# Kernel optimization log

Hardware: AMD Instinct MI355X
Metric: run time of the kernel (lower is better)

## Reference

```python
import jax, jax.numpy as jnp
import numpy as np

NUM_EXPERTS = 8
HIDDEN = 1024
INTER = 2048
TOKENS = 2048
TOP_K = 2


def setup_inputs() -> dict:
    key = jax.random.key(0)
    k1, k2, k3, k4, k5 = jax.random.split(key, 5)
    hidden_states = jax.random.normal(k1, (TOKENS, HIDDEN), dtype=jnp.float32)
    top_k_index = jax.random.randint(k2, (TOKENS, TOP_K), 0, NUM_EXPERTS, dtype=jnp.int64)
    top_k_weights = jax.random.uniform(k3, (TOKENS, TOP_K), dtype=jnp.float32)
    # parameters, scaled like typical init
    gate_up_proj = jax.random.normal(k4, (NUM_EXPERTS, 2 * INTER, HIDDEN), dtype=jnp.float32) * (HIDDEN ** -0.5)
    down_proj = jax.random.normal(k5, (NUM_EXPERTS, HIDDEN, INTER), dtype=jnp.float32) * (INTER ** -0.5)
    return {
        "hidden_states": hidden_states,
        "top_k_index": top_k_index,
        "top_k_weights": top_k_weights,
        "gate_up_proj": gate_up_proj,
        "down_proj": down_proj,
    }


def reference(hidden_states, top_k_index, top_k_weights, gate_up_proj, down_proj):
    # combine weights per (token, expert): w[t, e] = sum_k 1[idx[t,k]==e] * tw[t,k]
    one_hot = jax.nn.one_hot(top_k_index, NUM_EXPERTS, dtype=hidden_states.dtype)  # [T, K, E]
    combine = jnp.einsum("tke,tk->te", one_hot, top_k_weights)  # [T, E]

    out = jnp.zeros_like(hidden_states)
    # fixed small loop over experts (structural, not a data dim)
    for e in range(NUM_EXPERTS):
        gu = hidden_states @ gate_up_proj[e].T  # [T, 2I]
        gate, up = jnp.split(gu, 2, axis=-1)
        h = jax.nn.gelu(gate, approximate=True) * up  # gelu_pytorch_tanh
        y = h @ down_proj[e].T  # [T, H]
        out = out + y * combine[:, e][:, None]
    return out
```

## Files before the change

### kernel.cpp

```cpp
#include <hip/hip_runtime.h>
#include <stdint.h>

#define T_TOK  2048
#define HID    1024
#define INTERN 2048
#define NEXP   8
#define MAXPOS 5248

typedef __attribute__((ext_vector_type(8))) short          bf16x8;
typedef __attribute__((ext_vector_type(4))) float          f32x4;
typedef __attribute__((ext_vector_type(8))) unsigned short u16x8;
typedef __attribute__((ext_vector_type(4))) unsigned short u16x4;

__device__ __forceinline__ unsigned short f32_to_bf16(float f) {
  unsigned int u = __float_as_uint(f);
  unsigned int r = (u + 0x7FFFu + ((u >> 16) & 1u)) >> 16;
  return (unsigned short)r;
}

__device__ __forceinline__ float bf16_to_f32(unsigned short h) {
  unsigned int u = ((unsigned int)h) << 16;
  return __uint_as_float(u);
}

__device__ __forceinline__ void gload_lds16(const void* g, void* l) {
  __builtin_amdgcn_global_load_lds(
      (const __attribute__((address_space(1))) unsigned int*)g,
      (__attribute__((address_space(3))) unsigned int*)l, 16, 0, 0);
}

__device__ __forceinline__ u16x8 cvt8(float4 a, float4 b) {
  u16x8 w;
  w[0] = f32_to_bf16(a.x); w[1] = f32_to_bf16(a.y);
  w[2] = f32_to_bf16(a.z); w[3] = f32_to_bf16(a.w);
  w[4] = f32_to_bf16(b.x); w[5] = f32_to_bf16(b.y);
  w[6] = f32_to_bf16(b.z); w[7] = f32_to_bf16(b.w);
  return w;
}

#define WAIT_VM0()    asm volatile("s_waitcnt vmcnt(0)" ::: "memory")
#define WAIT_LGKM0()  asm volatile("s_waitcnt lgkmcnt(0)" ::: "memory")
#define SCHED_FENCE() __builtin_amdgcn_sched_barrier(0)

__global__ void route_kernel(const int* __restrict__ tki,
                             const float* __restrict__ tkw,
                             int* __restrict__ counts,
                             int* __restrict__ offsets,
                             int* __restrict__ tok_list,
                             float* __restrict__ w_list,
                             int* __restrict__ pos_map,
                             float* __restrict__ wgt_map) {
  __shared__ int scnt[NEXP];
  __shared__ int soff[NEXP];
  int tid = threadIdx.x;
  if (tid < NEXP) scnt[tid] = 0;
  __syncthreads();
  for (int t = tid; t < T_TOK; t += 256) {
    int e0 = tki[2 * t] & 7;
    int e1 = tki[2 * t + 1] & 7;
    float w0 = tkw[2 * t];
    float w1 = tkw[2 * t + 1];
    if (e0 == e1) {
      int p = atomicAdd(&scnt[e0], 1);
      tok_list[e0 * T_TOK + p] = t;
      w_list [e0 * T_TOK + p] = w0 + w1;
      pos_map[2 * t]     = (p << 3) | e0;
      wgt_map[2 * t]     = w0 + w1;
      pos_map[2 * t + 1] = -1;
      wgt_map[2 * t + 1] = 0.0f;
    } else {
      int p = atomicAdd(&scnt[e0], 1);
      tok_list[e0 * T_TOK + p] = t;
      w_list [e0 * T_TOK + p] = w0;
      pos_map[2 * t]     = (p << 3) | e0;
      wgt_map[2 * t]     = w0;
      int q = atomicAdd(&scnt[e1], 1);
      tok_list[e1 * T_TOK + q] = t;
      w_list [e1 * T_TOK + q] = w1;
      pos_map[2 * t + 1] = (q << 3) | e1;
      wgt_map[2 * t + 1] = w1;
    }
  }
  __syncthreads();
  if (tid == 0) {
    int acc = 0;
    for (int e = 0; e < NEXP; ++e) {
      counts[e]  = scnt[e];
      offsets[e] = acc;
      soff[e]    = acc;
      acc += ((scnt[e] + 127) >> 7) << 7;
    }
  }
  __syncthreads();
  for (int i = tid; i < 2 * T_TOK; i += 256) {
    int v = pos_map[i];
    if (v >= 0) pos_map[i] = soff[v & 7] + (v >> 3);
  }
}

__global__ void cvt_x_kernel(const float* __restrict__ x, unsigned short* __restrict__ xb) {
  int i = blockIdx.x * 256 + threadIdx.x;
  float4 v = ((const float4*)x)[i];
  u16x4 o;
  o[0] = f32_to_bf16(v.x); o[1] = f32_to_bf16(v.y);
  o[2] = f32_to_bf16(v.z); o[3] = f32_to_bf16(v.w);
  *((u16x4*)(xb + 4 * (size_t)i)) = o;
}

__global__ __launch_bounds__(256, 4)
void gemm1_kernel(const unsigned short* __restrict__ xb,
                  const float* __restrict__ gup,
                  const int* __restrict__ counts,
                  const int* __restrict__ offsets,
                  const int* __restrict__ tok_list,
                  unsigned short* __restrict__ hbuf) {
  int e  = blockIdx.z;
  int Ne = counts[e];
  int m0 = blockIdx.y * 128;
  if (m0 >= Ne) return;
  int n0  = blockIdx.x * 64;
  int off = offsets[e];

  __shared__ __align__(16) unsigned short As[2][4][128][8];
  __shared__ __align__(16) unsigned short Gs[2][4][64][8];
  __shared__ __align__(16) unsigned short Us[2][4][64][8];

  int tid  = threadIdx.x;
  int lane = tid & 63;
  int wave = tid >> 6;
  int wm = wave >> 1;
  int wn = wave & 1;

  int arow = tid & 127;
  int akg  = tid >> 7;
  int rg   = m0 + arow;
  int tok  = (rg < Ne) ? tok_list[e * T_TOK + rg] : 0;
  const unsigned short* asrc = xb + (size_t)tok * HID;

  int brow = tid >> 2;
  int bq   = tid & 3;
  const float* gsrc = gup + (size_t)e * (2 * INTERN) * HID + (size_t)(n0 + brow) * HID + bq * 8;
  const float* usrc = gsrc + (size_t)INTERN * HID;
  int brw = brow ^ bq;

  f32x4 accg[4][2], accu[4][2];
#pragma unroll
  for (int m = 0; m < 4; ++m)
#pragma unroll
    for (int n = 0; n < 2; ++n) {
      accg[m][n] = (f32x4){0.f, 0.f, 0.f, 0.f};
      accu[m][n] = (f32x4){0.f, 0.f, 0.f, 0.f};
    }

  float4 g0, g1, u0, u1;

  {
    const float4* gp = (const float4*)gsrc;
    const float4* up = (const float4*)usrc;
    g0 = gp[0]; g1 = gp[1];
    u0 = up[0]; u1 = up[1];
    char* base = (char*)&As[0][0][0][0];
    gload_lds16(asrc + akg * 8,       base + (size_t)tid * 16);
    gload_lds16(asrc + (akg + 2) * 8, base + 4096 + (size_t)tid * 16);
    *((u16x8*)&Gs[0][bq][brw][0]) = cvt8(g0, g1);
    *((u16x8*)&Us[0][bq][brw][0]) = cvt8(u0, u1);
    WAIT_LGKM0(); SCHED_FENCE();
  }

  int cur = 0;
  const int NT = HID / 32;
  for (int t = 0; t < NT; ++t) {
    WAIT_VM0(); SCHED_FENCE();
    __builtin_amdgcn_s_barrier(); SCHED_FENCE();
    int nxt = cur ^ 1;
    int kn = (t + 1 < NT) ? (t + 1) * 32 : 0;
    {
      const float4* gp = (const float4*)(gsrc + kn);
      const float4* up = (const float4*)(usrc + kn);
      g0 = gp[0]; g1 = gp[1];
      u0 = up[0]; u1 = up[1];
    }
    {
      char* base = (char*)&As[nxt][0][0][0];
      gload_lds16(asrc + kn + akg * 8,       base + (size_t)tid * 16);
      gload_lds16(asrc + kn + (akg + 2) * 8, base + 4096 + (size_t)tid * 16);
    }
    SCHED_FENCE();
    {
      int kg = lane >> 4;
      int rl = lane & 15;
      bf16x8 af[4], gf[2], uf[2];
#pragma unroll
      for (int m = 0; m < 4; ++m)
        af[m] = *((const bf16x8*)&As[cur][kg][wm * 64 + m * 16 + rl][0]);
#pragma unroll
      for (int n = 0; n < 2; ++n) {
        int r = (wn * 32 + n * 16 + rl) ^ kg;
        gf[n] = *((const bf16x8*)&Gs[cur][kg][r][0]);
        uf[n] = *((const bf16x8*)&Us[cur][kg][r][0]);
      }
#pragma unroll
      for (int m = 0; m < 4; ++m)
#pragma unroll
        for (int n = 0; n < 2; ++n) {
          accg[m][n] = __builtin_amdgcn_mfma_f32_16x16x32_bf16(af[m], gf[n], accg[m][n], 0, 0, 0);
          accu[m][n] = __builtin_amdgcn_mfma_f32_16x16x32_bf16(af[m], uf[n], accu[m][n], 0, 0, 0);
        }
    }
    *((u16x8*)&Gs[nxt][bq][brw][0]) = cvt8(g0, g1);
    *((u16x8*)&Us[nxt][bq][brw][0]) = cvt8(u0, u1);
    WAIT_LGKM0(); SCHED_FENCE();
    cur = nxt;
  }
  WAIT_VM0();

  int rl = lane & 15;
  int rq = lane >> 4;
  size_t hb_base = (size_t)((off + m0) >> 7) * (INTERN * 128);
#pragma unroll
  for (int m = 0; m < 4; ++m) {
#pragma unroll
    for (int n = 0; n < 2; ++n) {
      int col = n0 + wn * 32 + n * 16 + rl;
      size_t cbase = hb_base + (size_t)(col >> 3) * 1024 + (col & 7);
#pragma unroll
      for (int j = 0; j < 4; ++j) {
        int lr = wm * 64 + m * 16 + rq * 4 + j;
        if (m0 + lr < Ne) {
          float gv = accg[m][n][j];
          float uv = accu[m][n][j];
          float tt = gv + 0.044715f * gv * gv * gv;
          float a  = gv / (1.0f + __expf(-1.5957691216f * tt));
          hbuf[cbase + (size_t)lr * 8] = f32_to_bf16(a * uv);
        }
      }
    }
  }
}

__global__ __launch_bounds__(256, 2)
void gemm2_kernel(const unsigned short* __restrict__ hbuf,
                  const float* __restrict__ down,
                  const int* __restrict__ counts,
                  const int* __restrict__ offsets,
                  unsigned short* __restrict__ ybuf) {
  int e  = blockIdx.z;
  int Ne = counts[e];
  int m0 = blockIdx.y * 128;
  if (m0 >= Ne) return;
  int n0  = blockIdx.x * 64;
  int off = offsets[e];

  __shared__ __align__(16) unsigned short As[2][8][128][8];
  __shared__ __align__(16) unsigned short Bs[2][8][64][8];

  int tid  = threadIdx.x;
  int lane = tid & 63;
  int wave = tid >> 6;
  int wm = wave >> 1;
  int wn = wave & 1;

  const unsigned short* asrc = hbuf + (size_t)((off + m0) >> 7) * (INTERN * 128);

  int brow = tid >> 2;
  int bq   = tid & 3;
  int kgw0 = bq * 2, kgw1 = bq * 2 + 1;
  const float* bsrc = down + (size_t)e * HID * INTERN + (size_t)(n0 + brow) * INTERN + bq * 16;

  f32x4 acc[4][2];
#pragma unroll
  for (int m = 0; m < 4; ++m)
#pragma unroll
    for (int n = 0; n < 2; ++n) acc[m][n] = (f32x4){0.f, 0.f, 0.f, 0.f};

  float4 b0, b1, b2, b3;

  {
    const float4* bp = (const float4*)bsrc;
    b0 = bp[0]; b1 = bp[1]; b2 = bp[2]; b3 = bp[3];
    char* base = (char*)&As[0][0][0][0];
#pragma unroll
    for (int o = 0; o < 4; ++o)
      gload_lds16(asrc + o * 2048 + (size_t)tid * 8, base + o * 4096 + (size_t)tid * 16);
    *((u16x8*)&Bs[0][kgw0][brow ^ kgw0][0]) = cvt8(b0, b1);
    *((u16x8*)&Bs[0][kgw1][brow ^ kgw1][0]) = cvt8(b2, b3);
    WAIT_LGKM0(); SCHED_FENCE();
  }

  int cur = 0;
  const int NT = INTERN / 64;
  for (int t = 0; t < NT; ++t) {
    WAIT_VM0(); SCHED_FENCE();
    __builtin_amdgcn_s_barrier(); SCHED_FENCE();
    int nxt = cur ^ 1;
    int kn = (t + 1 < NT) ? (t + 1) * 64 : 0;
    {
      const float4* bp = (const float4*)(bsrc + kn);
      b0 = bp[0]; b1 = bp[1]; b2 = bp[2]; b3 = bp[3];
    }
    {
      char* base = (char*)&As[nxt][0][0][0];
      const unsigned short* ak = asrc + (size_t)kn * 128;
#pragma unroll
      for (int o = 0; o < 4; ++o)
        gload_lds16(ak + o * 2048 + (size_t)tid * 8, base + o * 4096 + (size_t)tid * 16);
    }
    SCHED_FENCE();
#pragma unroll
    for (int kk = 0; kk < 2; ++kk) {
      int kg = kk * 4 + (lane >> 4);
      int rl = lane & 15;
      bf16x8 af[4], bfv[2];
#pragma unroll
      for (int m = 0; m < 4; ++m)
        af[m] = *((const bf16x8*)&As[cur][kg][wm * 64 + m * 16 + rl][0]);
#pragma unroll
      for (int n = 0; n < 2; ++n)
        bfv[n] = *((const bf16x8*)&Bs[cur][kg][(wn * 32 + n * 16 + rl) ^ kg][0]);
#pragma unroll
      for (int m = 0; m < 4; ++m)
#pragma unroll
        for (int n = 0; n < 2; ++n)
          acc[m][n] = __builtin_amdgcn_mfma_f32_16x16x32_bf16(af[m], bfv[n], acc[m][n], 0, 0, 0);
    }
    *((u16x8*)&Bs[nxt][kgw0][brow ^ kgw0][0]) = cvt8(b0, b1);
    *((u16x8*)&Bs[nxt][kgw1][brow ^ kgw1][0]) = cvt8(b2, b3);
    WAIT_LGKM0(); SCHED_FENCE();
    cur = nxt;
  }
  WAIT_VM0();

  int rl = lane & 15;
  int rq = lane >> 4;
#pragma unroll
  for (int m = 0; m < 4; ++m) {
#pragma unroll
    for (int n = 0; n < 2; ++n) {
      int col = n0 + wn * 32 + n * 16 + rl;
#pragma unroll
      for (int j = 0; j < 4; ++j) {
        int lr = wm * 64 + m * 16 + rq * 4 + j;
        if (m0 + lr < Ne)
          ybuf[(size_t)(off + m0 + lr) * HID + col] = f32_to_bf16(acc[m][n][j]);
      }
    }
  }
}

__global__ void combine_kernel(const int* __restrict__ pos_map,
                               const float* __restrict__ wgt_map,
                               const unsigned short* __restrict__ ybuf,
                               float* __restrict__ out) {
  int i  = blockIdx.x * 256 + threadIdx.x;
  int t  = i >> 7;
  int c8 = i & 127;
  int p0 = pos_map[2 * t];
  int p1 = pos_map[2 * t + 1];
  float w0 = wgt_map[2 * t];
  float w1 = wgt_map[2 * t + 1];
  float acc[8];
#pragma unroll
  for (int j = 0; j < 8; ++j) acc[j] = 0.f;
  if (p0 >= 0) {
    u16x8 v = *((const u16x8*)(ybuf + (size_t)p0 * HID + c8 * 8));
#pragma unroll
    for (int j = 0; j < 8; ++j) acc[j] += w0 * bf16_to_f32(v[j]);
  }
  if (p1 >= 0) {
    u16x8 v = *((const u16x8*)(ybuf + (size_t)p1 * HID + c8 * 8));
#pragma unroll
    for (int j = 0; j < 8; ++j) acc[j] += w1 * bf16_to_f32(v[j]);
  }
  float4 o0 = make_float4(acc[0], acc[1], acc[2], acc[3]);
  float4 o1 = make_float4(acc[4], acc[5], acc[6], acc[7]);
  float4* dst = (float4*)(out + (size_t)t * HID + c8 * 8);
  dst[0] = o0;
  dst[1] = o1;
}

extern "C" void kernel_launch(void* const* d_in, const int* in_sizes, int n_in,
                              void* d_out, int out_size, void* d_ws, size_t ws_size,
                              hipStream_t stream) {
  (void)in_sizes; (void)n_in; (void)out_size;
  const float* hidden = (const float*)d_in[0];
  const int*   tki    = (const int*)d_in[1];
  const float* tkw    = (const float*)d_in[2];
  const float* gup    = (const float*)d_in[3];
  const float* down   = (const float*)d_in[4];
  float* out = (float*)d_out;
  char*  ws  = (char*)d_ws;

  int*   counts   = (int*)  (ws + 0);
  int*   offsets  = (int*)  (ws + 64);
  int*   tok_list = (int*)  (ws + 256);
  int*   pos_map  = (int*)  (ws + 65792);
  float* wgt_map  = (float*)(ws + 82176);
  float* w_list   = (float*)(ws + 98560);
  unsigned short* xb   = (unsigned short*)(ws + 164096);
  unsigned short* hbuf = (unsigned short*)(ws + 4358400);
  unsigned short* ybuf = (unsigned short*)(ws + 25854208);

  if (ws_size < 36602112ull) return;

  hipLaunchKernelGGL(route_kernel, dim3(1), dim3(256), 0, stream,
                     tki, tkw, counts, offsets, tok_list, w_list, pos_map, wgt_map);
  hipLaunchKernelGGL(cvt_x_kernel, dim3((T_TOK * HID / 4) / 256), dim3(256), 0, stream,
                     hidden, xb);
  hipLaunchKernelGGL(gemm1_kernel, dim3(INTERN / 64, T_TOK / 128, NEXP), dim3(256), 0, stream,
                     xb, gup, counts, offsets, tok_list, hbuf);
  hipLaunchKernelGGL(gemm2_kernel, dim3(HID / 64, T_TOK / 128, NEXP), dim3(256), 0, stream,
                     hbuf, down, counts, offsets, ybuf);
  hipLaunchKernelGGL(combine_kernel, dim3(T_TOK * HID / 8 / 256), dim3(256), 0, stream,
                     pos_map, wgt_map, ybuf, out);
}
```

Baseline: 143.7 us.

## Prefetch fp32 weights two tiles ahead and remap blocks for XCD locality

Both expert GEMMs now keep two register sets of fp32 weight loads and issue the global load two k-tiles ahead. They wait with vmcnt(4) instead of draining all outstanding loads each iteration, which is meant to hide weight-fetch latency behind the MFMA work. The grid is flattened to 1D and remapped so that blocks sharing the same expert and n-tile land on the same XCD, to improve L2 reuse of weight tiles. gemm1's launch bounds drop from 4 to 3 blocks per CU to leave room for the extra registers, which costs occupancy.

```diff
diff --git a/kernel.cpp b/kernel.cpp
--- a/kernel.cpp
+++ b/kernel.cpp
@@ -39,6 +39,7 @@
 }
 
 #define WAIT_VM0()    asm volatile("s_waitcnt vmcnt(0)" ::: "memory")
+#define WAIT_VM4()    asm volatile("s_waitcnt vmcnt(4)" ::: "memory")
 #define WAIT_LGKM0()  asm volatile("s_waitcnt lgkmcnt(0)" ::: "memory")
 #define SCHED_FENCE() __builtin_amdgcn_sched_barrier(0)
 
@@ -107,18 +108,65 @@
   *((u16x4*)(xb + 4 * (size_t)i)) = o;
 }
 
-__global__ __launch_bounds__(256, 4)
+#define G1_STEP(CUR, NXT, TILE, CG0, CG1, CU0, CU1, LG0, LG1, LU0, LU1)                            \
+  {                                                                                                \
+    WAIT_VM4(); SCHED_FENCE();                                                                     \
+    __builtin_amdgcn_s_barrier(); SCHED_FENCE();                                                   \
+    {                                                                                              \
+      int ka_ = ((TILE) + 1) * 32; if (ka_ >= HID) ka_ = 0;                                        \
+      char* base_ = (char*)&As[NXT][0][0][0];                                                      \
+      gload_lds16(asrc + ka_ + akg * 8,       base_ + (size_t)tid * 16);                           \
+      gload_lds16(asrc + ka_ + (akg + 2) * 8, base_ + 4096 + (size_t)tid * 16);                    \
+    }                                                                                              \
+    SCHED_FENCE();                                                                                 \
+    {                                                                                              \
+      int kb_ = ((TILE) + 2) * 32; if (kb_ >= HID) kb_ = 0;                                        \
+      const float4* gp_ = (const float4*)(gsrc + kb_);                                             \
+      const float4* up_ = (const float4*)(usrc + kb_);                                             \
+      LG0 = gp_[0]; LG1 = gp_[1]; LU0 = up_[0]; LU1 = up_[1];                                      \
+    }                                                                                              \
+    SCHED_FENCE();                                                                                 \
+    {                                                                                              \
+      int kg_ = lane >> 4;                                                                         \
+      int rl_ = lane & 15;                                                                         \
+      bf16x8 af[4], gf[2], uf[2];                                                                  \
+      for (int m = 0; m < 4; ++m)                                                                  \
+        af[m] = *((const bf16x8*)&As[CUR][kg_][wm * 64 + m * 16 + rl_][0]);                        \
+      for (int n = 0; n < 2; ++n) {                                                                \
+        int r_ = (wn * 32 + n * 16 + rl_) ^ kg_;                                                   \
+        gf[n] = *((const bf16x8*)&Gs[CUR][kg_][r_][0]);                                            \
+        uf[n] = *((const bf16x8*)&Us[CUR][kg_][r_][0]);                                            \
+      }                                                                                            \
+      for (int m = 0; m < 4; ++m)                                                                  \
+        for (int n = 0; n < 2; ++n) {                                                              \
+          accg[m][n] = __builtin_amdgcn_mfma_f32_16x16x32_bf16(af[m], gf[n], accg[m][n], 0, 0, 0); \
+          accu[m][n] = __builtin_amdgcn_mfma_f32_16x16x32_bf16(af[m], uf[n], accu[m][n], 0, 0, 0); \
+        }                                                                                          \
+    }                                                                                              \
+    *((u16x8*)&Gs[NXT][bq][brw][0]) = cvt8(CG0, CG1);                                              \
+    *((u16x8*)&Us[NXT][bq][brw][0]) = cvt8(CU0, CU1);                                              \
+    WAIT_LGKM0(); SCHED_FENCE();                                                                   \
+  }
+
+__global__ __launch_bounds__(256, 3)
 void gemm1_kernel(const unsigned short* __restrict__ xb,
                   const float* __restrict__ gup,
                   const int* __restrict__ counts,
                   const int* __restrict__ offsets,
                   const int* __restrict__ tok_list,
                   unsigned short* __restrict__ hbuf) {
-  int e  = blockIdx.z;
+  int lid = blockIdx.x;
+  int xcd = lid & 7;
+  int k2  = lid >> 3;
+  int ne  = xcd * 32 + (k2 >> 4);
+  int mq  = k2 & 15;
+  int nb  = ne & 31;
+  int e   = ne >> 5;
+
   int Ne = counts[e];
-  int m0 = blockIdx.y * 128;
+  int m0 = mq * 128;
   if (m0 >= Ne) return;
-  int n0  = blockIdx.x * 64;
+  int n0  = nb * 64;
   int off = offsets[e];
 
   __shared__ __align__(16) unsigned short As[2][4][128][8];
@@ -152,65 +200,28 @@
       accu[m][n] = (f32x4){0.f, 0.f, 0.f, 0.f};
     }
 
-  float4 g0, g1, u0, u1;
+  float4 xg0, xg1, xu0, xu1;
+  float4 yg0, yg1, yu0, yu1;
 
   {
-    const float4* gp = (const float4*)gsrc;
-    const float4* up = (const float4*)usrc;
-    g0 = gp[0]; g1 = gp[1];
-    u0 = up[0]; u1 = up[1];
     char* base = (char*)&As[0][0][0][0];
     gload_lds16(asrc + akg * 8,       base + (size_t)tid * 16);
     gload_lds16(asrc + (akg + 2) * 8, base + 4096 + (size_t)tid * 16);
-    *((u16x8*)&Gs[0][bq][brw][0]) = cvt8(g0, g1);
-    *((u16x8*)&Us[0][bq][brw][0]) = cvt8(u0, u1);
+    const float4* gp = (const float4*)gsrc;
+    const float4* up = (const float4*)usrc;
+    float4 tg0 = gp[0], tg1 = gp[1], tu0 = up[0], tu1 = up[1];
+    *((u16x8*)&Gs[0][bq][brw][0]) = cvt8(tg0, tg1);
+    *((u16x8*)&Us[0][bq][brw][0]) = cvt8(tu0, tu1);
+    const float4* gp1 = (const float4*)(gsrc + 32);
+    const float4* up1 = (const float4*)(usrc + 32);
+    yg0 = gp1[0]; yg1 = gp1[1]; yu0 = up1[0]; yu1 = up1[1];
     WAIT_LGKM0(); SCHED_FENCE();
   }
 
-  int cur = 0;
   const int NT = HID / 32;
-  for (int t = 0; t < NT; ++t) {
-    WAIT_VM0(); SCHED_FENCE();
-    __builtin_amdgcn_s_barrier(); SCHED_FENCE();
-    int nxt = cur ^ 1;
-    int kn = (t + 1 < NT) ? (t + 1) * 32 : 0;
-    {
-      const float4* gp = (const float4*)(gsrc + kn);
-      const float4* up = (const float4*)(usrc + kn);
-      g0 = gp[0]; g1 = gp[1];
-      u0 = up[0]; u1 = up[1];
-    }
-    {
-      char* base = (char*)&As[nxt][0][0][0];
-      gload_lds16(asrc + kn + akg * 8,       base + (size_t)tid * 16);
-      gload_lds16(asrc + kn + (akg + 2) * 8, base + 4096 + (size_t)tid * 16);
-    }
-    SCHED_FENCE();
-    {
-      int kg = lane >> 4;
-      int rl = lane & 15;
-      bf16x8 af[4], gf[2], uf[2];
-#pragma unroll
-      for (int m = 0; m < 4; ++m)
-        af[m] = *((const bf16x8*)&As[cur][kg][wm * 64 + m * 16 + rl][0]);
-#pragma unroll
-      for (int n = 0; n < 2; ++n) {
-        int r = (wn * 32 + n * 16 + rl) ^ kg;
-        gf[n] = *((const bf16x8*)&Gs[cur][kg][r][0]);
-        uf[n] = *((const bf16x8*)&Us[cur][kg][r][0]);
-      }
-#pragma unroll
-      for (int m = 0; m < 4; ++m)
-#pragma unroll
-        for (int n = 0; n < 2; ++n) {
-          accg[m][n] = __builtin_amdgcn_mfma_f32_16x16x32_bf16(af[m], gf[n], accg[m][n], 0, 0, 0);
-          accu[m][n] = __builtin_amdgcn_mfma_f32_16x16x32_bf16(af[m], uf[n], accu[m][n], 0, 0, 0);
-        }
-    }
-    *((u16x8*)&Gs[nxt][bq][brw][0]) = cvt8(g0, g1);
-    *((u16x8*)&Us[nxt][bq][brw][0]) = cvt8(u0, u1);
-    WAIT_LGKM0(); SCHED_FENCE();
-    cur = nxt;
+  for (int tt = 0; tt < NT; tt += 2) {
+    G1_STEP(0, 1, tt,     yg0, yg1, yu0, yu1,  xg0, xg1, xu0, xu1);
+    G1_STEP(1, 0, tt + 1, xg0, xg1, xu0, xu1,  yg0, yg1, yu0, yu1);
   }
   WAIT_VM0();
 
@@ -229,14 +240,49 @@
         if (m0 + lr < Ne) {
           float gv = accg[m][n][j];
           float uv = accu[m][n][j];
-          float tt = gv + 0.044715f * gv * gv * gv;
-          float a  = gv / (1.0f + __expf(-1.5957691216f * tt));
+          float tt2 = gv + 0.044715f * gv * gv * gv;
+          float a  = gv / (1.0f + __expf(-1.5957691216f * tt2));
           hbuf[cbase + (size_t)lr * 8] = f32_to_bf16(a * uv);
         }
       }
     }
   }
 }
+
+#define G2_STEP(CUR, NXT, TILE, CB0, CB1, CB2, CB3, LB0, LB1, LB2, LB3)                            \
+  {                                                                                                \
+    WAIT_VM4(); SCHED_FENCE();                                                                     \
+    __builtin_amdgcn_s_barrier(); SCHED_FENCE();                                                   \
+    {                                                                                              \
+      int ka_ = ((TILE) + 1) * 64; if (ka_ >= INTERN) ka_ = 0;                                     \
+      char* base_ = (char*)&As[NXT][0][0][0];                                                      \
+      const unsigned short* ak_ = asrc + (size_t)ka_ * 128;                                        \
+      for (int o = 0; o < 4; ++o)                                                                  \
+        gload_lds16(ak_ + o * 2048 + (size_t)tid * 8, base_ + o * 4096 + (size_t)tid * 16);        \
+    }                                                                                              \
+    SCHED_FENCE();                                                                                 \
+    {                                                                                              \
+      int kb_ = ((TILE) + 2) * 64; if (kb_ >= INTERN) kb_ = 0;                                     \
+      const float4* bp_ = (const float4*)(bsrc + kb_);                                             \
+      LB0 = bp_[0]; LB1 = bp_[1]; LB2 = bp_[2]; LB3 = bp_[3];                                      \
+    }                                                                                              \
+    SCHED_FENCE();                                                                                 \
+    for (int kk = 0; kk < 2; ++kk) {                                                               \
+      int kg_ = kk * 4 + (lane >> 4);                                                              \
+      int rl_ = lane & 15;                                                                         \
+      bf16x8 af[4], bfv[2];                                                                        \
+      for (int m = 0; m < 4; ++m)                                                                  \
+        af[m] = *((const bf16x8*)&As[CUR][kg_][wm * 64 + m * 16 + rl_][0]);                        \
+      for (int n = 0; n < 2; ++n)                                                                  \
+        bfv[n] = *((const bf16x8*)&Bs[CUR][kg_][(wn * 32 + n * 16 + rl_) ^ kg_][0]);               \
+      for (int m = 0; m < 4; ++m)                                                                  \
+        for (int n = 0; n < 2; ++n)                                                                \
+          acc[m][n] = __builtin_amdgcn_mfma_f32_16x16x32_bf16(af[m], bfv[n], acc[m][n], 0, 0, 0);  \
+    }                                                                                              \
+    *((u16x8*)&Bs[NXT][kgw0][brow ^ kgw0][0]) = cvt8(CB0, CB1);                                    \
+    *((u16x8*)&Bs[NXT][kgw1][brow ^ kgw1][0]) = cvt8(CB2, CB3);                                    \
+    WAIT_LGKM0(); SCHED_FENCE();                                                                   \
+  }
 
 __global__ __launch_bounds__(256, 2)
 void gemm2_kernel(const unsigned short* __restrict__ hbuf,
@@ -244,11 +290,18 @@
                   const int* __restrict__ counts,
                   const int* __restrict__ offsets,
                   unsigned short* __restrict__ ybuf) {
-  int e  = blockIdx.z;
+  int lid = blockIdx.x;
+  int xcd = lid & 7;
+  int k2  = lid >> 3;
+  int ne  = xcd * 16 + (k2 >> 4);
+  int mq  = k2 & 15;
+  int nb  = ne & 15;
+  int e   = ne >> 4;
+
   int Ne = counts[e];
-  int m0 = blockIdx.y * 128;
+  int m0 = mq * 128;
   if (m0 >= Ne) return;
-  int n0  = blockIdx.x * 64;
+  int n0  = nb * 64;
   int off = offsets[e];
 
   __shared__ __align__(16) unsigned short As[2][8][128][8];
@@ -273,60 +326,27 @@
 #pragma unroll
     for (int n = 0; n < 2; ++n) acc[m][n] = (f32x4){0.f, 0.f, 0.f, 0.f};
 
-  float4 b0, b1, b2, b3;
+  float4 xb0, xb1, xb2, xb3;
+  float4 yb0, yb1, yb2, yb3;
 
   {
-    const float4* bp = (const float4*)bsrc;
-    b0 = bp[0]; b1 = bp[1]; b2 = bp[2]; b3 = bp[3];
     char* base = (char*)&As[0][0][0][0];
 #pragma unroll
     for (int o = 0; o < 4; ++o)
       gload_lds16(asrc + o * 2048 + (size_t)tid * 8, base + o * 4096 + (size_t)tid * 16);
-    *((u16x8*)&Bs[0][kgw0][brow ^ kgw0][0]) = cvt8(b0, b1);
-    *((u16x8*)&Bs[0][kgw1][brow ^ kgw1][0]) = cvt8(b2, b3);
+    const float4* bp = (const float4*)bsrc;
+    float4 t0 = bp[0], t1 = bp[1], t2 = bp[2], t3 = bp[3];
+    *((u16x8*)&Bs[0][kgw0][brow ^ kgw0][0]) = cvt8(t0, t1);
+    *((u16x8*)&Bs[0][kgw1][brow ^ kgw1][0]) = cvt8(t2, t3);
+    const float4* bp1 = (const float4*)(bsrc + 64);
+    yb0 = bp1[0]; yb1 = bp1[1]; yb2 = bp1[2]; yb3 = bp1[3];
     WAIT_LGKM0(); SCHED_FENCE();
   }
 
-  int cur = 0;
   const int NT = INTERN / 64;
-  for (int t = 0; t < NT; ++t) {
-    WAIT_VM0(); SCHED_FENCE();
-    __builtin_amdgcn_s_barrier(); SCHED_FENCE();
-    int nxt = cur ^ 1;
-    int kn = (t + 1 < NT) ? (t + 1) * 64 : 0;
-    {
-      const float4* bp = (const float4*)(bsrc + kn);
-      b0 = bp[0]; b1 = bp[1]; b2 = bp[2]; b3 = bp[3];
-    }
-    {
-      char* base = (char*)&As[nxt][0][0][0];
-      const unsigned short* ak = asrc + (size_t)kn * 128;
-#pragma unroll
-      for (int o = 0; o < 4; ++o)
-        gload_lds16(ak + o * 2048 + (size_t)tid * 8, base + o * 4096 + (size_t)tid * 16);
-    }
-    SCHED_FENCE();
-#pragma unroll
-    for (int kk = 0; kk < 2; ++kk) {
-      int kg = kk * 4 + (lane >> 4);
-      int rl = lane & 15;
-      bf16x8 af[4], bfv[2];
-#pragma unroll
-      for (int m = 0; m < 4; ++m)
-        af[m] = *((const bf16x8*)&As[cur][kg][wm * 64 + m * 16 + rl][0]);
-#pragma unroll
-      for (int n = 0; n < 2; ++n)
-        bfv[n] = *((const bf16x8*)&Bs[cur][kg][(wn * 32 + n * 16 + rl) ^ kg][0]);
-#pragma unroll
-      for (int m = 0; m < 4; ++m)
-#pragma unroll
-        for (int n = 0; n < 2; ++n)
-          acc[m][n] = __builtin_amdgcn_mfma_f32_16x16x32_bf16(af[m], bfv[n], acc[m][n], 0, 0, 0);
-    }
-    *((u16x8*)&Bs[nxt][kgw0][brow ^ kgw0][0]) = cvt8(b0, b1);
-    *((u16x8*)&Bs[nxt][kgw1][brow ^ kgw1][0]) = cvt8(b2, b3);
-    WAIT_LGKM0(); SCHED_FENCE();
-    cur = nxt;
+  for (int tt = 0; tt < NT; tt += 2) {
+    G2_STEP(0, 1, tt,     yb0, yb1, yb2, yb3,  xb0, xb1, xb2, xb3);
+    G2_STEP(1, 0, tt + 1, xb0, xb1, xb2, xb3,  yb0, yb1, yb2, yb3);
   }
   WAIT_VM0();
 
@@ -406,9 +426,9 @@
                      tki, tkw, counts, offsets, tok_list, w_list, pos_map, wgt_map);
   hipLaunchKernelGGL(cvt_x_kernel, dim3((T_TOK * HID / 4) / 256), dim3(256), 0, stream,
                      hidden, xb);
-  hipLaunchKernelGGL(gemm1_kernel, dim3(INTERN / 64, T_TOK / 128, NEXP), dim3(256), 0, stream,
+  hipLaunchKernelGGL(gemm1_kernel, dim3(32 * 16 * NEXP), dim3(256), 0, stream,
                      xb, gup, counts, offsets, tok_list, hbuf);
-  hipLaunchKernelGGL(gemm2_kernel, dim3(HID / 64, T_TOK / 128, NEXP), dim3(256), 0, stream,
+  hipLaunchKernelGGL(gemm2_kernel, dim3(16 * 16 * NEXP), dim3(256), 0, stream,
                      hbuf, down, counts, offsets, ybuf);
   hipLaunchKernelGGL(combine_kernel, dim3(T_TOK * HID / 8 / 256), dim3(256), 0, stream,
                      pos_map, wgt_map, ybuf, out);
```

After: 155.0 us. 1.08x slower.

## Pre-gather routed tokens into a tiled contiguous buffer before gemm1

Applied to the files above, without the earlier changes.

Adds a gather kernel that copies each expert's routed token rows from the bf16 activations into a padded buffer laid out in 128-row tiles with k-group-major chunks. gemm1 then streams its A tile with contiguous, coalesced direct-to-LDS loads instead of per-row indirect gathers via tok_list. The goal is better memory coalescing in the main GEMM, at the cost of an extra kernel launch and an extra pass over roughly 10 MB of activations. The buffer aliases ybuf, which is fine because gemm2 only writes ybuf after gemm1 has consumed it.

```diff
diff --git a/kernel.cpp b/kernel.cpp
--- a/kernel.cpp
+++ b/kernel.cpp
@@ -107,12 +107,30 @@
   *((u16x4*)(xb + 4 * (size_t)i)) = o;
 }
 
+__global__ void gather_x_kernel(const unsigned short* __restrict__ xb,
+                                const int* __restrict__ counts,
+                                const int* __restrict__ offsets,
+                                const int* __restrict__ tok_list,
+                                unsigned short* __restrict__ xg) {
+  int p = blockIdx.x * 128 + threadIdx.x;
+  int c = blockIdx.y;
+  int e = 0;
+#pragma unroll
+  for (int k = 1; k < NEXP; ++k) if (p >= offsets[k]) e = k;
+  int r = p - offsets[e];
+  u16x8 v = (u16x8){0, 0, 0, 0, 0, 0, 0, 0};
+  if (r < counts[e]) {
+    int tok = tok_list[e * T_TOK + r];
+    v = *((const u16x8*)(xb + (size_t)tok * HID + c * 8));
+  }
+  *((u16x8*)(xg + (size_t)(p >> 7) * 131072 + c * 1024 + (p & 127) * 8)) = v;
+}
+
 __global__ __launch_bounds__(256, 4)
-void gemm1_kernel(const unsigned short* __restrict__ xb,
+void gemm1_kernel(const unsigned short* __restrict__ xg,
                   const float* __restrict__ gup,
                   const int* __restrict__ counts,
                   const int* __restrict__ offsets,
-                  const int* __restrict__ tok_list,
                   unsigned short* __restrict__ hbuf) {
   int e  = blockIdx.z;
   int Ne = counts[e];
@@ -131,11 +149,7 @@
   int wm = wave >> 1;
   int wn = wave & 1;
 
-  int arow = tid & 127;
-  int akg  = tid >> 7;
-  int rg   = m0 + arow;
-  int tok  = (rg < Ne) ? tok_list[e * T_TOK + rg] : 0;
-  const unsigned short* asrc = xb + (size_t)tok * HID;
+  const unsigned short* asrc = xg + (size_t)((off + m0) >> 7) * (HID * 128);
 
   int brow = tid >> 2;
   int bq   = tid & 3;
@@ -160,8 +174,8 @@
     g0 = gp[0]; g1 = gp[1];
     u0 = up[0]; u1 = up[1];
     char* base = (char*)&As[0][0][0][0];
-    gload_lds16(asrc + akg * 8,       base + (size_t)tid * 16);
-    gload_lds16(asrc + (akg + 2) * 8, base + 4096 + (size_t)tid * 16);
+    gload_lds16(asrc + (size_t)tid * 8,        base + (size_t)tid * 16);
+    gload_lds16(asrc + 2048 + (size_t)tid * 8, base + 4096 + (size_t)tid * 16);
     *((u16x8*)&Gs[0][bq][brw][0]) = cvt8(g0, g1);
     *((u16x8*)&Us[0][bq][brw][0]) = cvt8(u0, u1);
     WAIT_LGKM0(); SCHED_FENCE();
@@ -182,8 +196,9 @@
     }
     {
       char* base = (char*)&As[nxt][0][0][0];
-      gload_lds16(asrc + kn + akg * 8,       base + (size_t)tid * 16);
-      gload_lds16(asrc + kn + (akg + 2) * 8, base + 4096 + (size_t)tid * 16);
+      const unsigned short* ak = asrc + (size_t)kn * 128;
+      gload_lds16(ak + (size_t)tid * 8,        base + (size_t)tid * 16);
+      gload_lds16(ak + 2048 + (size_t)tid * 8, base + 4096 + (size_t)tid * 16);
     }
     SCHED_FENCE();
     {
@@ -229,8 +244,8 @@
         if (m0 + lr < Ne) {
           float gv = accg[m][n][j];
           float uv = accu[m][n][j];
-          float tt = gv + 0.044715f * gv * gv * gv;
-          float a  = gv / (1.0f + __expf(-1.5957691216f * tt));
+          float tt2 = gv + 0.044715f * gv * gv * gv;
+          float a  = gv / (1.0f + __expf(-1.5957691216f * tt2));
           hbuf[cbase + (size_t)lr * 8] = f32_to_bf16(a * uv);
         }
       }
@@ -399,6 +414,7 @@
   unsigned short* xb   = (unsigned short*)(ws + 164096);
   unsigned short* hbuf = (unsigned short*)(ws + 4358400);
   unsigned short* ybuf = (unsigned short*)(ws + 25854208);
+  unsigned short* xg   = ybuf;
 
   if (ws_size < 36602112ull) return;
 
@@ -406,8 +422,10 @@
                      tki, tkw, counts, offsets, tok_list, w_list, pos_map, wgt_map);
   hipLaunchKernelGGL(cvt_x_kernel, dim3((T_TOK * HID / 4) / 256), dim3(256), 0, stream,
                      hidden, xb);
+  hipLaunchKernelGGL(gather_x_kernel, dim3(MAXPOS / 128, 128), dim3(128), 0, stream,
+                     xb, counts, offsets, tok_list, xg);
   hipLaunchKernelGGL(gemm1_kernel, dim3(INTERN / 64, T_TOK / 128, NEXP), dim3(256), 0, stream,
-                     xb, gup, counts, offsets, tok_list, hbuf);
+                     xg, gup, counts, offsets, hbuf);
   hipLaunchKernelGGL(gemm2_kernel, dim3(HID / 64, T_TOK / 128, NEXP), dim3(256), 0, stream,
                      hbuf, down, counts, offsets, ybuf);
   hipLaunchKernelGGL(combine_kernel, dim3(T_TOK * HID / 8 / 256), dim3(256), 0, stream,
```

Result: slower. 148.5 us (+3.3%).
